# Kernel tuning notes

Hardware: AMD Instinct MI355X
Metric: run time of the kernel (lower is better)

## Reference

```python
import jax, jax.numpy as jnp
import numpy as np


def setup_inputs() -> dict:
    key = jax.random.key(0)
    ks = jax.random.split(key, 5)
    b, t, q_dim, kv_dim, h = 16, 128, 256, 64, 4
    c = t - 1
    q_x = jax.random.normal(ks[0], (b, t, q_dim), dtype=jnp.float32)
    kv_x = jax.random.normal(ks[1], (b, t, c, kv_dim), dtype=jnp.float32)
    # Linear weights stored as [in, out]; no biases (bias=False in torch module).
    sq = 1.0 / np.sqrt(q_dim)
    sk = 1.0 / np.sqrt(kv_dim)
    Wq = jax.random.uniform(ks[2], (q_dim, kv_dim * h), jnp.float32, -sq, sq)
    Wk = jax.random.uniform(ks[3], (kv_dim, kv_dim * h), jnp.float32, -sk, sk)
    Wv = jax.random.uniform(ks[4], (kv_dim, kv_dim * h), jnp.float32, -sk, sk)
    return {"q_x": q_x, "kv_x": kv_x, "Wq": Wq, "Wk": Wk, "Wv": Wv}


def reference(q_x, kv_x, Wq, Wk, Wv):
    b, t, c, k = kv_x.shape  # c = t - 1
    h = Wq.shape[1] // k
    # projections
    q = (q_x @ Wq).reshape(b, t, h, k)          # [b,t,h,k]
    keys = (kv_x @ Wk).reshape(b, t, c, h, k)   # [b,t,c,h,k]
    vals = (kv_x @ Wv).reshape(b, t, c, h, k)
    # per-token attention over the c-sized context
    scores = jnp.einsum('bthk,btchk->bthc', q, keys) / jnp.sqrt(jnp.float32(k))
    w = jax.nn.softmax(scores, axis=-1)          # softmax over context dim
    out = jnp.einsum('bthc,btchk->bthk', w, vals)
    return out.reshape(b, t, h * k)
```

## Files before the change

kernel.cpp:

```cpp
#include <hip/hip_runtime.h>
#include <math.h>

#define Bdim 16
#define Tdim 128
#define Cdim 127
#define Hdim 4
#define QD   256
#define HK   256
#define BT   (Bdim * Tdim)

#define DPP_XOR1        0xB1
#define DPP_XOR2        0x4E
#define DPP_HALF_MIRROR 0x141
#define DPP_MIRROR      0x140
template<int CTRL>
__device__ __forceinline__ float dpp_movf(float x) {
    return __int_as_float(__builtin_amdgcn_update_dpp(
        0, __float_as_int(x), CTRL, 0xF, 0xF, true));
}
__device__ __forceinline__ float quad_sum(float v) {
    v += dpp_movf<DPP_XOR1>(v);
    v += dpp_movf<DPP_XOR2>(v);
    return v;
}
__device__ __forceinline__ float rows_sum(float v) {
    v += dpp_movf<DPP_HALF_MIRROR>(v);
    v += dpp_movf<DPP_MIRROR>(v);
    v += __shfl_xor(v, 16, 64);
    v += __shfl_xor(v, 32, 64);
    return v;
}
__device__ __forceinline__ float wx_red(float v) {
    v += dpp_movf<DPP_XOR1>(v);
    v += dpp_movf<DPP_XOR2>(v);
    v += dpp_movf<DPP_HALF_MIRROR>(v);
    v += dpp_movf<DPP_MIRROR>(v);
    v += __shfl_xor(v, 16, 64);
    return v;
}

__global__ __launch_bounds__(256) void qk_fused(
        const float* __restrict__ q_x,
        const float* __restrict__ Wq,
        const float* __restrict__ Wk,
        float* __restrict__ qk) {
    __shared__ __align__(16) float q_s[4][256];
    __shared__ __align__(16) float p_s[4][4][68];
    int RB = blockIdx.x;
    int tid = threadIdx.x;
    {
        int r = tid >> 6, kq = tid & 63;
        *(float4*)&q_s[r][kq*4] =
            *(const float4*)(q_x + (size_t)(RB*4 + r) * QD + kq * 4);
    }
    __syncthreads();

    float acc[4] = {0.f, 0.f, 0.f, 0.f};
    #pragma unroll 4
    for (int i4 = 0; i4 < 64; ++i4) {
        float w0 = Wq[(size_t)(4*i4+0) * HK + tid];
        float w1 = Wq[(size_t)(4*i4+1) * HK + tid];
        float w2 = Wq[(size_t)(4*i4+2) * HK + tid];
        float w3 = Wq[(size_t)(4*i4+3) * HK + tid];
        #pragma unroll
        for (int r = 0; r < 4; ++r) {
            float4 qv = *(const float4*)&q_s[r][i4*4];
            acc[r] = fmaf(qv.x, w0, fmaf(qv.y, w1, fmaf(qv.z, w2, fmaf(qv.w, w3, acc[r]))));
        }
    }
    int h = tid >> 6, m = tid & 63;
    #pragma unroll
    for (int r = 0; r < 4; ++r) p_s[r][h][m] = acc[r];
    __syncthreads();

    const float4* wk4 = (const float4*)(Wk + (size_t)m * HK + h * 64);
    float4 wkr[16];
    #pragma unroll
    for (int j = 0; j < 16; ++j) wkr[j] = wk4[j];
    float a2[4] = {0.f, 0.f, 0.f, 0.f};
    #pragma unroll
    for (int j4 = 0; j4 < 16; ++j4) {
        #pragma unroll
        for (int r = 0; r < 4; ++r) {
            float4 pv = *(const float4*)&p_s[r][h][j4*4];
            a2[r] = fmaf(pv.x, wkr[j4].x, fmaf(pv.y, wkr[j4].y,
                    fmaf(pv.z, wkr[j4].z, fmaf(pv.w, wkr[j4].w, a2[r]))));
        }
    }
    #pragma unroll
    for (int r = 0; r < 4; ++r)
        qk[(size_t)(RB*4 + r) * HK + tid] = a2[r];
}

__global__ __launch_bounds__(512, 6) void attn_main(
        const float* __restrict__ kv_x,
        const float* __restrict__ qk_g,
        const float* __restrict__ Wv,
        float* __restrict__ out) {
    __shared__ __align__(16) float4 sX4[128 * 16];
    __shared__ __align__(16) float qk_s[HK];
    __shared__ __align__(16) float4 e4[128];
    __shared__ __align__(16) float4 wx4[Hdim * 16];
    __shared__ __align__(16) float4 reds[8];

    int bt  = blockIdx.x;
    int tid = threadIdx.x;

    const float4* Xg = (const float4*)(kv_x + (size_t)bt * (Cdim * 64));
    #pragma unroll
    for (int it = 0; it < 4; ++it) {
        int l = tid + it * 512;
        if (l < Cdim * 16) {
            int c = l >> 4, p = l & 15;
            __builtin_amdgcn_global_load_lds(
                (const __attribute__((address_space(1))) void*)(Xg + (c << 4) + (p ^ (c & 7))),
                (__attribute__((address_space(3))) void*)(sX4 + l), 16, 0, 0);
        }
    }
    if (tid >= 256 && tid < 320)
        ((float*)sX4)[Cdim * 64 + (tid - 256)] = 0.f;
    if (tid < 256)
        qk_s[tid] = qk_g[(size_t)bt * HK + tid];
    __syncthreads();

    int lane = tid & 63;
    int wave = tid >> 6;
    int c  = tid >> 2;
    int qp = tid & 3;
    int sw = c & 7;

    float e0, e1, e2, e3;
    {
        const float4* xrow = sX4 + c * 16;
        float4 x0 = xrow[(qp*4 + 0) ^ sw];
        float4 x1 = xrow[(qp*4 + 1) ^ sw];
        float4 x2 = xrow[(qp*4 + 2) ^ sw];
        float4 x3 = xrow[(qp*4 + 3) ^ sw];
        const float4* qk4 = (const float4*)qk_s;
        float a0 = 0.f, a1 = 0.f, a2 = 0.f, a3 = 0.f;
        #pragma unroll
        for (int i = 0; i < 4; ++i) {
            float4 xi = (i == 0) ? x0 : (i == 1) ? x1 : (i == 2) ? x2 : x3;
            float4 q0 = qk4[0*16 + qp*4 + i];
            float4 q1 = qk4[1*16 + qp*4 + i];
            float4 q2 = qk4[2*16 + qp*4 + i];
            float4 q3 = qk4[3*16 + qp*4 + i];
            a0 = fmaf(q0.x, xi.x, fmaf(q0.y, xi.y, fmaf(q0.z, xi.z, fmaf(q0.w, xi.w, a0))));
            a1 = fmaf(q1.x, xi.x, fmaf(q1.y, xi.y, fmaf(q1.z, xi.z, fmaf(q1.w, xi.w, a1))));
            a2 = fmaf(q2.x, xi.x, fmaf(q2.y, xi.y, fmaf(q2.z, xi.z, fmaf(q2.w, xi.w, a2))));
            a3 = fmaf(q3.x, xi.x, fmaf(q3.y, xi.y, fmaf(q3.z, xi.z, fmaf(q3.w, xi.w, a3))));
        }
        a0 = quad_sum(a0); a1 = quad_sum(a1); a2 = quad_sum(a2); a3 = quad_sum(a3);
        bool valid = (c < Cdim);
        e0 = valid ? __expf(a0 * 0.125f) : 0.f;
        e1 = valid ? __expf(a1 * 0.125f) : 0.f;
        e2 = valid ? __expf(a2 * 0.125f) : 0.f;
        e3 = valid ? __expf(a3 * 0.125f) : 0.f;
    }
    if (qp == 0) e4[c] = make_float4(e0, e1, e2, e3);
    float t0 = rows_sum(e0), t1 = rows_sum(e1), t2 = rows_sum(e2), t3 = rows_sum(e3);
    if (lane == 0) reds[wave] = make_float4(t0, t1, t2, t3);
    __syncthreads();

    {
        int jc = tid >> 5;
        int mq = (lane >> 3) & 3;
        int cs = lane & 7;
        float4 A0 = {0,0,0,0}, A1 = {0,0,0,0}, A2 = {0,0,0,0}, A3 = {0,0,0,0};
        #pragma unroll
        for (int mm = 0; mm < 4; ++mm) {
            int cc = cs + 8 * (mq * 4 + mm);
            float4 x4 = sX4[cc * 16 + (jc ^ cs)];
            float4 ee = e4[cc];
            A0.x = fmaf(ee.x, x4.x, A0.x); A0.y = fmaf(ee.x, x4.y, A0.y);
            A0.z = fmaf(ee.x, x4.z, A0.z); A0.w = fmaf(ee.x, x4.w, A0.w);
            A1.x = fmaf(ee.y, x4.x, A1.x); A1.y = fmaf(ee.y, x4.y, A1.y);
            A1.z = fmaf(ee.y, x4.z, A1.z); A1.w = fmaf(ee.y, x4.w, A1.w);
            A2.x = fmaf(ee.z, x4.x, A2.x); A2.y = fmaf(ee.z, x4.y, A2.y);
            A2.z = fmaf(ee.z, x4.z, A2.z); A2.w = fmaf(ee.z, x4.w, A2.w);
            A3.x = fmaf(ee.w, x4.x, A3.x); A3.y = fmaf(ee.w, x4.y, A3.y);
            A3.z = fmaf(ee.w, x4.z, A3.z); A3.w = fmaf(ee.w, x4.w, A3.w);
        }
        A0.x = wx_red(A0.x); A0.y = wx_red(A0.y); A0.z = wx_red(A0.z); A0.w = wx_red(A0.w);
        A1.x = wx_red(A1.x); A1.y = wx_red(A1.y); A1.z = wx_red(A1.z); A1.w = wx_red(A1.w);
        A2.x = wx_red(A2.x); A2.y = wx_red(A2.y); A2.z = wx_red(A2.z); A2.w = wx_red(A2.w);
        A3.x = wx_red(A3.x); A3.y = wx_red(A3.y); A3.z = wx_red(A3.z); A3.w = wx_red(A3.w);
        if ((lane & 31) == 0) {
            wx4[0 * 16 + jc] = A0;
            wx4[1 * 16 + jc] = A1;
            wx4[2 * 16 + jc] = A2;
            wx4[3 * 16 + jc] = A3;
        }
    }
    __syncthreads();

    if (tid < 256) {
        int hh = tid >> 6, k = tid & 63;
        float4 sums = reds[0];
        #pragma unroll
        for (int w = 1; w < 8; ++w) {
            float4 r = reds[w];
            sums.x += r.x; sums.y += r.y; sums.z += r.z; sums.w += r.w;
        }
        float denom = (hh == 0) ? sums.x : (hh == 1) ? sums.y
                    : (hh == 2) ? sums.z : sums.w;
        float inv = 1.f / denom;
        const float* wvcol = Wv + hh * 64 + k;
        float acc = 0.f;
        #pragma unroll 4
        for (int jc = 0; jc < 16; ++jc) {
            float4 w4 = wx4[hh * 16 + jc];
            acc = fmaf(w4.x, wvcol[(size_t)(jc*4+0) * HK],
                  fmaf(w4.y, wvcol[(size_t)(jc*4+1) * HK],
                  fmaf(w4.z, wvcol[(size_t)(jc*4+2) * HK],
                  fmaf(w4.w, wvcol[(size_t)(jc*4+3) * HK], acc))));
        }
        out[(size_t)bt * HK + tid] = acc * inv;
    }
}

extern "C" void kernel_launch(void* const* d_in, const int* in_sizes, int n_in,
                              void* d_out, int out_size, void* d_ws, size_t ws_size,
                              hipStream_t stream) {
    const float* q_x  = (const float*)d_in[0];
    const float* kv_x = (const float*)d_in[1];
    const float* Wq   = (const float*)d_in[2];
    const float* Wk   = (const float*)d_in[3];
    const float* Wv   = (const float*)d_in[4];
    float* out = (float*)d_out;

    float* qk = (float*)d_ws;

    qk_fused<<<BT / 4, 256, 0, stream>>>(q_x, Wq, Wk, qk);
    attn_main<<<BT, 512, 0, stream>>>(kv_x, qk, Wv, out);
}
```

Before: 39.11 us.

## Read kv_x directly from global memory instead of staging in LDS

Removes the shared-memory staging buffer for the per-token kv_x tile and has both the score phase and the weighted-sum phase load kv_x from global memory. Padding rows are clamped to row 0, and their softmax weights are zero. The freed LDS allows raising the occupancy hint from 6 to 8 blocks per CU. In exchange each element is fetched twice from global memory, and the second pass depends on cache hits with a strided access pattern.

```diff
diff --git a/kernel.cpp b/kernel.cpp
--- a/kernel.cpp
+++ b/kernel.cpp
@@ -92,12 +92,11 @@
         qk[(size_t)(RB*4 + r) * HK + tid] = a2[r];
 }
 
-__global__ __launch_bounds__(512, 6) void attn_main(
+__global__ __launch_bounds__(512, 8) void attn_main(
         const float* __restrict__ kv_x,
         const float* __restrict__ qk_g,
         const float* __restrict__ Wv,
         float* __restrict__ out) {
-    __shared__ __align__(16) float4 sX4[128 * 16];
     __shared__ __align__(16) float qk_s[HK];
     __shared__ __align__(16) float4 e4[128];
     __shared__ __align__(16) float4 wx4[Hdim * 16];
@@ -105,20 +104,8 @@
 
     int bt  = blockIdx.x;
     int tid = threadIdx.x;
-
-    const float4* Xg = (const float4*)(kv_x + (size_t)bt * (Cdim * 64));
-    #pragma unroll
-    for (int it = 0; it < 4; ++it) {
-        int l = tid + it * 512;
-        if (l < Cdim * 16) {
-            int c = l >> 4, p = l & 15;
-            __builtin_amdgcn_global_load_lds(
-                (const __attribute__((address_space(1))) void*)(Xg + (c << 4) + (p ^ (c & 7))),
-                (__attribute__((address_space(3))) void*)(sX4 + l), 16, 0, 0);
-        }
-    }
-    if (tid >= 256 && tid < 320)
-        ((float*)sX4)[Cdim * 64 + (tid - 256)] = 0.f;
+    const float* Xr = kv_x + (size_t)bt * (Cdim * 64);
+
     if (tid < 256)
         qk_s[tid] = qk_g[(size_t)bt * HK + tid];
     __syncthreads();
@@ -127,15 +114,16 @@
     int wave = tid >> 6;
     int c  = tid >> 2;
     int qp = tid & 3;
-    int sw = c & 7;
 
     float e0, e1, e2, e3;
     {
-        const float4* xrow = sX4 + c * 16;
-        float4 x0 = xrow[(qp*4 + 0) ^ sw];
-        float4 x1 = xrow[(qp*4 + 1) ^ sw];
-        float4 x2 = xrow[(qp*4 + 2) ^ sw];
-        float4 x3 = xrow[(qp*4 + 3) ^ sw];
+        bool valid = (c < Cdim);
+        int crow = valid ? c : 0;
+        const float4* xq = (const float4*)(Xr + crow * 64) + qp * 4;
+        float4 x0 = xq[0];
+        float4 x1 = xq[1];
+        float4 x2 = xq[2];
+        float4 x3 = xq[3];
         const float4* qk4 = (const float4*)qk_s;
         float a0 = 0.f, a1 = 0.f, a2 = 0.f, a3 = 0.f;
         #pragma unroll
@@ -151,7 +139,6 @@
             a3 = fmaf(q3.x, xi.x, fmaf(q3.y, xi.y, fmaf(q3.z, xi.z, fmaf(q3.w, xi.w, a3))));
         }
         a0 = quad_sum(a0); a1 = quad_sum(a1); a2 = quad_sum(a2); a3 = quad_sum(a3);
-        bool valid = (c < Cdim);
         e0 = valid ? __expf(a0 * 0.125f) : 0.f;
         e1 = valid ? __expf(a1 * 0.125f) : 0.f;
         e2 = valid ? __expf(a2 * 0.125f) : 0.f;
@@ -170,7 +157,8 @@
         #pragma unroll
         for (int mm = 0; mm < 4; ++mm) {
             int cc = cs + 8 * (mq * 4 + mm);
-            float4 x4 = sX4[cc * 16 + (jc ^ cs)];
+            int ccrow = (cc < Cdim) ? cc : 0;
+            float4 x4 = *(const float4*)(Xr + ccrow * 64 + jc * 4);
             float4 ee = e4[cc];
             A0.x = fmaf(ee.x, x4.x, A0.x); A0.y = fmaf(ee.x, x4.y, A0.y);
             A0.z = fmaf(ee.x, x4.z, A0.z); A0.w = fmaf(ee.x, x4.w, A0.w);
```

Measured after the change: 42.76 us. 1.09x slower.
